# Performance work log

Hardware: AMD Instinct MI355X
Metric: run time of the kernel (lower is better)

The kernel has to match this reference:

```python
import jax, jax.numpy as jnp
import numpy as np

B, S, D, H, OUT = 64, 512, 128, 512, 24


def _linear_params(key, out_dim, in_dim, dtype=jnp.float32):
    kw, kb = jax.random.split(key)
    bound = 1.0 / np.sqrt(in_dim)
    w = jax.random.uniform(kw, (out_dim, in_dim), dtype, -bound, bound)
    b = jax.random.uniform(kb, (out_dim,), dtype, -bound, bound)
    return w, b


def setup_inputs() -> dict:
    key = jax.random.key(0)
    ks = jax.random.split(key, 12)
    inp = {"x": jax.random.normal(ks[0], (B, S, D), jnp.float32)}
    # layer 0 gates: Linear(D+H, H); layer 1 gates: Linear(2H, H)
    names = ["f", "i", "o", "g"]
    for li, in_dim in enumerate([D + H, 2 * H]):
        for gi, n in enumerate(names):
            w, b = _linear_params(ks[1 + li * 4 + gi], H, in_dim)
            inp[f"w{n}{li}"] = w
            inp[f"b{n}{li}"] = b
    inp["fc1_w"], inp["fc1_b"] = _linear_params(ks[9], H, H)
    inp["fc2_w"], inp["fc2_b"] = _linear_params(ks[10], OUT, H)
    return inp


def _cell(inp, h, c, wf, bf, wi, bi, wo, bo, wg, bg):
    comb = jnp.concatenate([inp, h], axis=1)          # [B, in+H]
    f = jax.nn.sigmoid(comb @ wf.T + bf)
    i = jax.nn.sigmoid(comb @ wi.T + bi)
    g = jnp.tanh(comb @ wg.T + bg)
    c = f * c + i * g
    o = jax.nn.sigmoid(comb @ wo.T + bo)
    h = o * jnp.tanh(c)
    return h, c


def reference(x, wf0, bf0, wi0, bi0, wo0, bo0, wg0, bg0,
              wf1, bf1, wi1, bi1, wo1, bo1, wg1, bg1,
              fc1_w, fc1_b, fc2_w, fc2_b):
    layers = ((wf0, bf0, wi0, bi0, wo0, bo0, wg0, bg0),
              (wf1, bf1, wi1, bi1, wo1, bo1, wg1, bg1))
    b, h = x.shape[0], bf0.shape[0]

    def step(carry, xt):
        new = []
        inp = xt
        for params, (hs, cs) in zip(layers, carry):
            hs, cs = _cell(inp, hs, cs, *params)
            inp = hs
            new.append((hs, cs))
        return tuple(new), inp  # last layer's hidden

    init = tuple((jnp.zeros((b, h), x.dtype), jnp.zeros((b, h), x.dtype))
                 for _ in range(len(layers)))
    _, outs = jax.lax.scan(step, init, jnp.swapaxes(x, 0, 1))  # outs: [S, B, H]
    last = outs[-1]                                            # h at final t
    out = last @ fc1_w.T + fc1_b                               # dropout is eval-mode identity
    out = out @ fc2_w.T + fc2_b
    return jax.nn.relu(out)
```

## Files before the change

### kernel.cpp

```cpp
#include <hip/hip_runtime.h>
#include <cmath>

constexpr int kB = 64, kS = 512, kD = 128, kH = 512, kOut = 24;
constexpr int kBlocks = 256, kThreads = 512;
constexpr size_t kBarOffBytes = (size_t)5 * kB * kH * 4;

struct Params {
  const float* x;
  const float* w0[4]; const float* b0[4];
  const float* w1[4]; const float* b1[4];
  const float* fc1w; const float* fc1b;
  const float* fc2w; const float* fc2b;
  float* H0;
  float* H1;
  float* tmp1;
  unsigned* bar;
  float* out;
};

__device__ __forceinline__ float sigmoidf_(float v) {
  return 1.0f / (1.0f + expf(-v));
}

__device__ __forceinline__ void sync_group(unsigned* slots, unsigned* gen,
                                           int myIdx, int n, bool leader,
                                           unsigned r) {
  const int tid = threadIdx.x;
  __syncthreads();
  if (leader) {
    if (tid == 0) {
      __threadfence();
      __hip_atomic_store(slots + myIdx * 16, r + 1, __ATOMIC_RELAXED,
                         __HIP_MEMORY_SCOPE_AGENT);
    }
    unsigned* ps = slots + (tid < n ? tid : 0) * 16;
    for (;;) {
      unsigned v = __hip_atomic_load(ps, __ATOMIC_RELAXED,
                                     __HIP_MEMORY_SCOPE_AGENT);
      if (__syncthreads_and((tid < n) ? (int)(v > r) : 1)) break;
      __builtin_amdgcn_s_sleep(1);
    }
    __threadfence();
    if (tid == 0)
      __hip_atomic_store(gen, r + 1, __ATOMIC_RELAXED,
                         __HIP_MEMORY_SCOPE_AGENT);
    __syncthreads();
  } else {
    if (tid == 0) {
      __threadfence();
      __hip_atomic_store(slots + myIdx * 16, r + 1, __ATOMIC_RELAXED,
                         __HIP_MEMORY_SCOPE_AGENT);
      while (__hip_atomic_load(gen, __ATOMIC_RELAXED,
                               __HIP_MEMORY_SCOPE_AGENT) <= r)
        __builtin_amdgcn_s_sleep(1);
      __threadfence();
    }
    __syncthreads();
  }
}

__global__ void __launch_bounds__(kThreads, 2)
lstm_persistent(Params p) {
  __shared__ float wlds0[16 * 644];
  __shared__ float wlds1[16 * 1028];
  __shared__ float blds[32];

  const int tid = threadIdx.x;
  const int bid = blockIdx.x;
  const int cgi = bid >> 1;
  const int bh  = bid & 1;
  const int j0  = cgi * 4;
  const int bbase = bh * 32;

  const int wv = tid >> 6;
  const int l  = tid & 63;
  const int kt = l & 15;
  const int bi = l >> 4;
  const int bme = bbase + wv * 4 + bi;

  for (int idx = tid; idx < 16 * 160; idx += kThreads) {
    const int row = idx / 160;
    const int k4  = idx - row * 160;
    *(float4*)(wlds0 + row * 644 + k4 * 4) =
        *(const float4*)(p.w0[row >> 2] + (j0 + (row & 3)) * 640 + k4 * 4);
  }
  for (int idx = tid; idx < 16 * 256; idx += kThreads) {
    const int row = idx >> 8;
    const int k4  = idx & 255;
    *(float4*)(wlds1 + row * 1028 + k4 * 4) =
        *(const float4*)(p.w1[row >> 2] + (j0 + (row & 3)) * 1024 + k4 * 4);
  }
  if (tid < 16)       blds[tid] = p.b0[tid >> 2][j0 + (tid & 3)];
  else if (tid < 32)  blds[tid] = p.b1[(tid - 16) >> 2][j0 + (tid & 3)];

  if (tid < 128) {
    const int jl = tid >> 5, bb = tid & 31;
    const int b = bbase + bb;
    p.H0[kB * kH + b * kH + j0 + jl] = 0.f;
    p.H1[kB * kH + b * kH + j0 + jl] = 0.f;
  }

  float* H0buf[2] = { p.H0, p.H0 + kB * kH };
  float* H1buf[2] = { p.H1, p.H1 + kB * kH };
  float c0[4] = {0.f, 0.f, 0.f, 0.f};
  float c1[4] = {0.f, 0.f, 0.f, 0.f};

  unsigned* domSlots = p.bar + bh * 2048;
  unsigned* domGen   = p.bar + 4096 + bh * 16;
  const bool leader  = (cgi == 0);
  unsigned rnd = 0;

  sync_group(domSlots, domGen, cgi, 128, leader, rnd); rnd++;

  auto runPhase = [&](int C, auto&& src, const float* __restrict__ wl,
                      int wstride, const float* __restrict__ bl,
                      float* cs, float* __restrict__ hout) {
    float acc[16];
    #pragma unroll
    for (int r2 = 0; r2 < 16; ++r2) acc[r2] = 0.f;

    auto compute = [&](int c, const float4 u0, const float4 u1) {
      #pragma unroll
      for (int r2 = 0; r2 < 16; ++r2) {
        const float* wr = wl + r2 * wstride + c * 128;
        const float4 w0q = *(const float4*)(wr + kt * 4);
        const float4 w1q = *(const float4*)(wr + 64 + kt * 4);
        float a = acc[r2];
        a = fmaf(w0q.x, u0.x, a); a = fmaf(w0q.y, u0.y, a);
        a = fmaf(w0q.z, u0.z, a); a = fmaf(w0q.w, u0.w, a);
        a = fmaf(w1q.x, u1.x, a); a = fmaf(w1q.y, u1.y, a);
        a = fmaf(w1q.z, u1.z, a); a = fmaf(w1q.w, u1.w, a);
        acc[r2] = a;
      }
    };

    float4 uA0 = *(const float4*)src(0, bme, kt);
    float4 uA1 = *(const float4*)src(0, bme, 16 + kt);
    float4 uB0, uB1;
    if (C > 1) {
      uB0 = *(const float4*)src(1, bme, kt);
      uB1 = *(const float4*)src(1, bme, 16 + kt);
    }

    for (int cc = 0; cc < C; cc += 2) {
      {
        const int c = cc;
        const float4 d0 = uA0, d1 = uA1;
        if (c + 2 < C) {
          uA0 = *(const float4*)src(c + 2, bme, kt);
          uA1 = *(const float4*)src(c + 2, bme, 16 + kt);
        }
        compute(c, d0, d1);
      }
      if (cc + 1 < C) {
        const int c = cc + 1;
        const float4 d0 = uB0, d1 = uB1;
        if (c + 2 < C) {
          uB0 = *(const float4*)src(c + 2, bme, kt);
          uB1 = *(const float4*)src(c + 2, bme, 16 + kt);
        }
        compute(c, d0, d1);
      }
    }

    #pragma unroll
    for (int r2 = 0; r2 < 16; ++r2) {
      float v = acc[r2];
      v += __shfl_xor(v, 1, 64);
      v += __shfl_xor(v, 2, 64);
      v += __shfl_xor(v, 4, 64);
      v += __shfl_xor(v, 8, 64);
      acc[r2] = v;
    }
    #pragma unroll
    for (int jl = 0; jl < 4; ++jl) {
      const float fg = sigmoidf_(acc[0 * 4 + jl] + bl[0 * 4 + jl]);
      const float ig = sigmoidf_(acc[1 * 4 + jl] + bl[1 * 4 + jl]);
      const float og = sigmoidf_(acc[2 * 4 + jl] + bl[2 * 4 + jl]);
      const float gg = tanhf(acc[3 * 4 + jl] + bl[3 * 4 + jl]);
      cs[jl] = fg * cs[jl] + ig * gg;
      const float hv = og * tanhf(cs[jl]);
      if (kt == 0) hout[bme * kH + j0 + jl] = hv;
    }
  };

  {
    const float* __restrict__ h0prev = H0buf[1];
    auto srcA = [&](int c, int b, int q4) {
      return (c == 0) ? p.x + (b * kS + 0) * kD + q4 * 4
                      : h0prev + b * kH + (c - 1) * 128 + q4 * 4;
    };
    runPhase(5, srcA, wlds0, 644, &blds[0], c0, H0buf[0]);
  }
  sync_group(domSlots, domGen, cgi, 128, leader, rnd); rnd++;

  for (int t = 0; t < kS; ++t) {
    {
      const float* __restrict__ h0cur  = H0buf[t & 1];
      const float* __restrict__ h1prev = H1buf[(t + 1) & 1];
      auto srcB = [&](int c, int b, int q4) {
        return (c < 4) ? h0cur + b * kH + c * 128 + q4 * 4
                       : h1prev + b * kH + (c - 4) * 128 + q4 * 4;
      };
      runPhase(8, srcB, wlds1, 1028, &blds[16], c1, H1buf[t & 1]);
    }
    if (t < kS - 1) {
      const int tn = t + 1;
      const float* __restrict__ h0prev = H0buf[t & 1];
      auto srcA = [&](int c, int b, int q4) {
        return (c == 0) ? p.x + (b * kS + tn) * kD + q4 * 4
                        : h0prev + b * kH + (c - 1) * 128 + q4 * 4;
      };
      runPhase(5, srcA, wlds0, 644, &blds[0], c0, H0buf[(t + 1) & 1]);
    }
    sync_group(domSlots, domGen, cgi, 128, leader, rnd); rnd++;
  }

  const float* h1f = H1buf[(kS - 1) & 1];
  if (tid < 128) {
    const int jl = tid >> 5, bb = tid & 31;
    const int b = bbase + bb;
    const float* __restrict__ wrr = p.fc1w + (j0 + jl) * kH;
    const float* __restrict__ hr = h1f + b * kH;
    float s = p.fc1b[j0 + jl];
    for (int k = 0; k < kH; k += 4) {
      const float4 wv4 = *(const float4*)(wrr + k);
      const float4 hv = *(const float4*)(hr + k);
      s = fmaf(wv4.x, hv.x, s); s = fmaf(wv4.y, hv.y, s);
      s = fmaf(wv4.z, hv.z, s); s = fmaf(wv4.w, hv.w, s);
    }
    p.tmp1[b * kH + j0 + jl] = s;
  }
  sync_group(p.bar + 4224, p.bar + 8320, bid, 256, bid == 0, 0u);

  if (bid < kOut && tid < kB) {
    const int b = tid;
    const float* __restrict__ wrr = p.fc2w + bid * kH;
    const float* __restrict__ tr = p.tmp1 + b * kH;
    float s = p.fc2b[bid];
    for (int k = 0; k < kH; k += 4) {
      const float4 wv4 = *(const float4*)(wrr + k);
      const float4 tv = *(const float4*)(tr + k);
      s = fmaf(wv4.x, tv.x, s); s = fmaf(wv4.y, tv.y, s);
      s = fmaf(wv4.z, tv.z, s); s = fmaf(wv4.w, tv.w, s);
    }
    p.out[b * kOut + bid] = fmaxf(s, 0.f);
  }
}

extern "C" void kernel_launch(void* const* d_in, const int* in_sizes, int n_in,
                              void* d_out, int out_size, void* d_ws, size_t ws_size,
                              hipStream_t stream) {
  (void)in_sizes; (void)n_in; (void)out_size; (void)ws_size;
  Params p;
  p.x = (const float*)d_in[0];
  p.w0[0] = (const float*)d_in[1];  p.b0[0] = (const float*)d_in[2];
  p.w0[1] = (const float*)d_in[3];  p.b0[1] = (const float*)d_in[4];
  p.w0[2] = (const float*)d_in[5];  p.b0[2] = (const float*)d_in[6];
  p.w0[3] = (const float*)d_in[7];  p.b0[3] = (const float*)d_in[8];
  p.w1[0] = (const float*)d_in[9];  p.b1[0] = (const float*)d_in[10];
  p.w1[1] = (const float*)d_in[11]; p.b1[1] = (const float*)d_in[12];
  p.w1[2] = (const float*)d_in[13]; p.b1[2] = (const float*)d_in[14];
  p.w1[3] = (const float*)d_in[15]; p.b1[3] = (const float*)d_in[16];
  p.fc1w = (const float*)d_in[17];  p.fc1b = (const float*)d_in[18];
  p.fc2w = (const float*)d_in[19];  p.fc2b = (const float*)d_in[20];

  float* ws = (float*)d_ws;
  p.H0   = ws;
  p.H1   = ws + 2 * kB * kH;
  p.tmp1 = ws + 4 * kB * kH;
  p.bar  = (unsigned*)((char*)d_ws + kBarOffBytes);
  p.out  = (float*)d_out;

  hipMemsetAsync((char*)d_ws + kBarOffBytes, 0, 36864, stream);

  void* args[] = { &p };
  hipLaunchCooperativeKernel(reinterpret_cast<const void*>(&lstm_persistent),
                             dim3(kBlocks), dim3(kThreads), args, 0, stream);
}
```

Measured before the change: 14.43 ms.

## Remap LSTM gate GEMV lanes to 4x4 register tile over batch and hidden units

Changes the per-wave thread mapping so each lane computes four gates for one hidden unit across four batch rows, instead of sixteen gate rows for one batch row. Each weight float4 loaded from LDS is now reused across four batch inputs, cutting LDS traffic per FMA. The cost is more input float4s held in registers (16 instead of 4 prefetched), higher register pressure and a wider cross-lane reduction. The cell state now tracks batch rows per lane rather than hidden units.

```diff
diff --git a/kernel.cpp b/kernel.cpp
--- a/kernel.cpp
+++ b/kernel.cpp
@@ -74,9 +74,9 @@
 
   const int wv = tid >> 6;
   const int l  = tid & 63;
-  const int kt = l & 15;
-  const int bi = l >> 4;
-  const int bme = bbase + wv * 4 + bi;
+  const int kt = l >> 2;
+  const int ci = l & 3;
+  const int bw0 = bbase + wv * 4;
 
   for (int idx = tid; idx < 16 * 160; idx += kThreads) {
     const int row = idx / 160;
@@ -115,72 +115,92 @@
   auto runPhase = [&](int C, auto&& src, const float* __restrict__ wl,
                       int wstride, const float* __restrict__ bl,
                       float* cs, float* __restrict__ hout) {
-    float acc[16];
+    float acc[4][4];
     #pragma unroll
-    for (int r2 = 0; r2 < 16; ++r2) acc[r2] = 0.f;
-
-    auto compute = [&](int c, const float4 u0, const float4 u1) {
+    for (int g = 0; g < 4; ++g)
       #pragma unroll
-      for (int r2 = 0; r2 < 16; ++r2) {
-        const float* wr = wl + r2 * wstride + c * 128;
-        const float4 w0q = *(const float4*)(wr + kt * 4);
-        const float4 w1q = *(const float4*)(wr + 64 + kt * 4);
-        float a = acc[r2];
-        a = fmaf(w0q.x, u0.x, a); a = fmaf(w0q.y, u0.y, a);
-        a = fmaf(w0q.z, u0.z, a); a = fmaf(w0q.w, u0.w, a);
-        a = fmaf(w1q.x, u1.x, a); a = fmaf(w1q.y, u1.y, a);
-        a = fmaf(w1q.z, u1.z, a); a = fmaf(w1q.w, u1.w, a);
-        acc[r2] = a;
+      for (int bb = 0; bb < 4; ++bb) acc[g][bb] = 0.f;
+
+    auto compute = [&](int c, const float4* u8) {
+      #pragma unroll
+      for (int half = 0; half < 2; ++half) {
+        float4 wq[4];
+        #pragma unroll
+        for (int g = 0; g < 4; ++g)
+          wq[g] = *(const float4*)(wl + (g * 4 + ci) * wstride + c * 128 +
+                                   half * 64 + kt * 4);
+        #pragma unroll
+        for (int g = 0; g < 4; ++g)
+          #pragma unroll
+          for (int bb = 0; bb < 4; ++bb) {
+            const float4 u4 = u8[bb * 2 + half];
+            float a = acc[g][bb];
+            a = fmaf(wq[g].x, u4.x, a); a = fmaf(wq[g].y, u4.y, a);
+            a = fmaf(wq[g].z, u4.z, a); a = fmaf(wq[g].w, u4.w, a);
+            acc[g][bb] = a;
+          }
       }
     };
 
-    float4 uA0 = *(const float4*)src(0, bme, kt);
-    float4 uA1 = *(const float4*)src(0, bme, 16 + kt);
-    float4 uB0, uB1;
+    float4 uA[8], uB[8];
+    #pragma unroll
+    for (int q = 0; q < 8; ++q)
+      uA[q] = *(const float4*)src(0, bw0 + (q >> 1), (q & 1) * 16 + kt);
     if (C > 1) {
-      uB0 = *(const float4*)src(1, bme, kt);
-      uB1 = *(const float4*)src(1, bme, 16 + kt);
+      #pragma unroll
+      for (int q = 0; q < 8; ++q)
+        uB[q] = *(const float4*)src(1, bw0 + (q >> 1), (q & 1) * 16 + kt);
     }
 
     for (int cc = 0; cc < C; cc += 2) {
       {
         const int c = cc;
-        const float4 d0 = uA0, d1 = uA1;
+        float4 d[8];
+        #pragma unroll
+        for (int q = 0; q < 8; ++q) d[q] = uA[q];
         if (c + 2 < C) {
-          uA0 = *(const float4*)src(c + 2, bme, kt);
-          uA1 = *(const float4*)src(c + 2, bme, 16 + kt);
+          #pragma unroll
+          for (int q = 0; q < 8; ++q)
+            uA[q] = *(const float4*)src(c + 2, bw0 + (q >> 1),
+                                        (q & 1) * 16 + kt);
         }
-        compute(c, d0, d1);
+        compute(c, d);
       }
       if (cc + 1 < C) {
         const int c = cc + 1;
-        const float4 d0 = uB0, d1 = uB1;
+        float4 d[8];
+        #pragma unroll
+        for (int q = 0; q < 8; ++q) d[q] = uB[q];
         if (c + 2 < C) {
-          uB0 = *(const float4*)src(c + 2, bme, kt);
-          uB1 = *(const float4*)src(c + 2, bme, 16 + kt);
+          #pragma unroll
+          for (int q = 0; q < 8; ++q)
+            uB[q] = *(const float4*)src(c + 2, bw0 + (q >> 1),
+                                        (q & 1) * 16 + kt);
         }
-        compute(c, d0, d1);
+        compute(c, d);
       }
     }
 
     #pragma unroll
-    for (int r2 = 0; r2 < 16; ++r2) {
-      float v = acc[r2];
-      v += __shfl_xor(v, 1, 64);
-      v += __shfl_xor(v, 2, 64);
-      v += __shfl_xor(v, 4, 64);
-      v += __shfl_xor(v, 8, 64);
-      acc[r2] = v;
-    }
+    for (int g = 0; g < 4; ++g)
+      #pragma unroll
+      for (int bb = 0; bb < 4; ++bb) {
+        float v = acc[g][bb];
+        v += __shfl_xor(v, 4, 64);
+        v += __shfl_xor(v, 8, 64);
+        v += __shfl_xor(v, 16, 64);
+        v += __shfl_xor(v, 32, 64);
+        acc[g][bb] = v;
+      }
     #pragma unroll
-    for (int jl = 0; jl < 4; ++jl) {
-      const float fg = sigmoidf_(acc[0 * 4 + jl] + bl[0 * 4 + jl]);
-      const float ig = sigmoidf_(acc[1 * 4 + jl] + bl[1 * 4 + jl]);
-      const float og = sigmoidf_(acc[2 * 4 + jl] + bl[2 * 4 + jl]);
-      const float gg = tanhf(acc[3 * 4 + jl] + bl[3 * 4 + jl]);
-      cs[jl] = fg * cs[jl] + ig * gg;
-      const float hv = og * tanhf(cs[jl]);
-      if (kt == 0) hout[bme * kH + j0 + jl] = hv;
+    for (int bb = 0; bb < 4; ++bb) {
+      const float fg = sigmoidf_(acc[0][bb] + bl[0 * 4 + ci]);
+      const float ig = sigmoidf_(acc[1][bb] + bl[1 * 4 + ci]);
+      const float og = sigmoidf_(acc[2][bb] + bl[2 * 4 + ci]);
+      const float gg = tanhf(acc[3][bb] + bl[3 * 4 + ci]);
+      cs[bb] = fg * cs[bb] + ig * gg;
+      const float hv = og * tanhf(cs[bb]);
+      if (l < 4) hout[(bw0 + bb) * kH + j0 + ci] = hv;
     }
   };
 
```

Result: faster. 12.42 ms (-13.9%).
